# Kernel optimization log

Hardware: AMD Instinct MI355X
Metric: run time of the kernel (lower is better)

The kernel has to match this reference:

```python
import jax, jax.numpy as jnp
import numpy as np

EMBED_DIM = 1024
NUM_MEMORY_SLOTS = 256
B, Q = 8, 4096


def setup_inputs() -> dict:
    key = jax.random.key(0)
    ks = jax.random.split(key, 6)
    s = 1.0 / np.sqrt(EMBED_DIM)
    return {
        "x": jax.random.normal(ks[0], (B, Q, EMBED_DIM), dtype=jnp.float32),
        "memory_bank": jax.random.normal(ks[1], (NUM_MEMORY_SLOTS, EMBED_DIM), dtype=jnp.float32),
        "Wq": jax.random.uniform(ks[2], (EMBED_DIM, EMBED_DIM), jnp.float32, -s, s),
        "bq": jax.random.uniform(ks[3], (EMBED_DIM,), jnp.float32, -s, s),
        "Wo": jax.random.uniform(ks[4], (EMBED_DIM, EMBED_DIM), jnp.float32, -s, s),
        "bo": jax.random.uniform(ks[5], (EMBED_DIM,), jnp.float32, -s, s),
    }


def reference(x, memory_bank, Wq, bq, Wo, bo):
    # query projection: [B,Q,E]
    queries = jnp.einsum('bqe,fe->bqf', x, Wq) + bq
    # attention over fixed memory bank: scores [B,Q,M]
    scores = jnp.einsum('bqe,me->bqm', queries, memory_bank)
    weights = jax.nn.softmax(scores, axis=-1)
    attended = jnp.einsum('bqm,me->bqe', weights, memory_bank)
    # output projection + residual
    return jnp.einsum('bqe,fe->bqf', attended, Wo) + bo + x
```

## Files before the change

### kernel.cpp

```cpp
#include <hip/hip_runtime.h>
#include <hip/hip_bf16.h>
#include <stdint.h>

#define TOK 32768
#define EMB 1024
#define MSL 256

typedef __attribute__((ext_vector_type(8))) short short8;
typedef __attribute__((ext_vector_type(4))) float f32x4;

__device__ __forceinline__ ushort f2bf(float f) {
    union { float f; uint32_t u; } c; c.f = f;
    uint32_t u = c.u;
    return (ushort)((u + 0x7fffu + ((u >> 16) & 1u)) >> 16);
}

__device__ __forceinline__ void split2(float f, ushort& h, ushort& l) {
    union { float f; uint32_t u; } c; c.f = f;
    h = (ushort)(c.u >> 16);
    union { uint32_t u; float f; } hv; hv.u = c.u & 0xffff0000u;
    union { float f; uint32_t u; } lc; lc.f = f - hv.f;
    l = (ushort)(lc.u >> 16);
}

__device__ __forceinline__ void async_copy16(const void* gsrc, void* ldst) {
    __builtin_amdgcn_global_load_lds(
        (const __attribute__((address_space(1))) uint32_t*)gsrc,
        (__attribute__((address_space(3))) uint32_t*)ldst,
        16, 0, 0);
}


__global__ __launch_bounds__(256) void pre_small(
    const float* __restrict__ Wq, ushort* __restrict__ wqth, ushort* __restrict__ wqtl,
    const float* __restrict__ mb, ushort* __restrict__ mbh, ushort* __restrict__ mbl,
    const float* __restrict__ bq, float* __restrict__ cvec)
{
    __shared__ float ld[64 * 65];
    const int b = blockIdx.x;
    const int t = threadIdx.x;
    if (b < 256) {
        const int eBase = (b & 15) * 64;
        const int fBase = (b >> 4) * 64;
        #pragma unroll
        for (int r = 0; r < 16; ++r) {
            int row = r * 4 + (t >> 6);
            int col = t & 63;
            ld[row * 65 + col] = Wq[(size_t)(fBase + row) * EMB + eBase + col];
        }
        __syncthreads();
        #pragma unroll
        for (int r = 0; r < 16; ++r) {
            int row = r * 4 + (t >> 6);
            int col = t & 63;
            float v = ld[col * 65 + row];
            ushort h, l; split2(v, h, l);
            size_t o = (size_t)(eBase + row) * EMB + fBase + col;
            wqth[o] = h; wqtl[o] = l;
        }
    } else if (b < 512) {
        int i = (b - 256) * 256 + t;
        float4 v = ((const float4*)mb)[i];
        ushort4 h4, l4;
        split2(v.x, h4.x, l4.x); split2(v.y, h4.y, l4.y);
        split2(v.z, h4.z, l4.z); split2(v.w, h4.w, l4.w);
        ((ushort4*)mbh)[i] = h4;
        ((ushort4*)mbl)[i] = l4;
    } else {
        int m = (b - 512) * 4 + (t >> 6);
        int lane = t & 63;
        const float4* mrow = (const float4*)(mb + (size_t)m * EMB);
        const float4* brow = (const float4*)bq;
        float s = 0.f;
        #pragma unroll
        for (int k = 0; k < 4; ++k) {
            float4 a = mrow[lane + k * 64];
            float4 bb = brow[lane + k * 64];
            s += a.x * bb.x + a.y * bb.y + a.z * bb.z + a.w * bb.w;
        }
        #pragma unroll
        for (int off = 32; off; off >>= 1) s += __shfl_xor(s, off, 64);
        if (lane == 0) cvec[m] = s;
    }
}

template<int MODE>
__device__ __forceinline__ void gemm_body(
    ushort* smem, const float* __restrict__ A,
    const ushort* __restrict__ Bh, const ushort* __restrict__ Bl,
    ushort* __restrict__ O1, ushort* __restrict__ O2,
    int K, int ldc, int bx, int by)
{
    ushort* sAh = smem;
    ushort* sAl = smem + 8192;
    ushort* sBh = smem + 16384;
    ushort* sBl = smem + 24576;

    const int t = threadIdx.x;
    const int lane = t & 63;
    const int wave = t >> 6;
    const int wr = wave >> 1;
    const int wc = wave & 1;
    const int rowBase = by * 128;
    const int colBase = bx * 128;

    const float*  Ab  = A  + (size_t)rowBase * K;
    const ushort* Bhb = Bh + (size_t)colBase * K;
    const ushort* Blb = Bl + (size_t)colBase * K;

    const int cg = ((t & 7) ^ ((t >> 3) & 7)) << 3;

    f32x4 acc[4][4] = {};

    const int kIters = K >> 6;
    for (int kt = 0; kt < kIters; ++kt) {
        const int k0 = kt << 6;
        __syncthreads();
        #pragma unroll
        for (int r = 0; r < 4; ++r) {
            int row = r * 32 + (t >> 3);
            async_copy16(Bhb + (size_t)row * K + k0 + cg, &sBh[(size_t)(r * 256 + wave * 64) * 8]);
            async_copy16(Blb + (size_t)row * K + k0 + cg, &sBl[(size_t)(r * 256 + wave * 64) * 8]);
        }
        #pragma unroll
        for (int r = 0; r < 4; ++r) {
            int i = r * 256 + t;
            int row = r * 32 + (t >> 3);
            const float* src = Ab + (size_t)row * K + k0 + cg;
            float4 f0 = *(const float4*)src;
            float4 f1 = *(const float4*)(src + 4);
            short8 hv, lv; ushort h, l;
            split2(f0.x, h, l); hv[0] = (short)h; lv[0] = (short)l;
            split2(f0.y, h, l); hv[1] = (short)h; lv[1] = (short)l;
            split2(f0.z, h, l); hv[2] = (short)h; lv[2] = (short)l;
            split2(f0.w, h, l); hv[3] = (short)h; lv[3] = (short)l;
            split2(f1.x, h, l); hv[4] = (short)h; lv[4] = (short)l;
            split2(f1.y, h, l); hv[5] = (short)h; lv[5] = (short)l;
            split2(f1.z, h, l); hv[6] = (short)h; lv[6] = (short)l;
            split2(f1.w, h, l); hv[7] = (short)h; lv[7] = (short)l;
            *(short8*)&sAh[(size_t)i * 8] = hv;
            *(short8*)&sAl[(size_t)i * 8] = lv;
        }
        __syncthreads();

        #pragma unroll
        for (int ks = 0; ks < 2; ++ks) {
            const int kc = ks * 4 + (lane >> 4);
            short8 ah[4], al[4], bh[4], bl[4];
            #pragma unroll
            for (int i2 = 0; i2 < 4; ++i2) {
                int row = wr * 64 + i2 * 16 + (lane & 15);
                int off = row * 64 + ((kc ^ (row & 7)) << 3);
                ah[i2] = *(const short8*)&sAh[off];
                al[i2] = *(const short8*)&sAl[off];
            }
            #pragma unroll
            for (int j = 0; j < 4; ++j) {
                int row = wc * 64 + j * 16 + (lane & 15);
                int off = row * 64 + ((kc ^ (row & 7)) << 3);
                bh[j] = *(const short8*)&sBh[off];
                bl[j] = *(const short8*)&sBl[off];
            }
            #pragma unroll
            for (int i2 = 0; i2 < 4; ++i2)
                #pragma unroll
                for (int j = 0; j < 4; ++j) {
                    acc[i2][j] = __builtin_amdgcn_mfma_f32_16x16x32_bf16(ah[i2], bh[j], acc[i2][j], 0, 0, 0);
                    acc[i2][j] = __builtin_amdgcn_mfma_f32_16x16x32_bf16(ah[i2], bl[j], acc[i2][j], 0, 0, 0);
                    acc[i2][j] = __builtin_amdgcn_mfma_f32_16x16x32_bf16(al[i2], bh[j], acc[i2][j], 0, 0, 0);
                }
        }
    }

    #pragma unroll
    for (int i2 = 0; i2 < 4; ++i2) {
        #pragma unroll
        for (int j = 0; j < 4; ++j) {
            const int col = colBase + wc * 64 + j * 16 + (lane & 15);
            #pragma unroll
            for (int r = 0; r < 4; ++r) {
                const int row = rowBase + wr * 64 + i2 * 16 + ((lane >> 4) << 2) + r;
                float v = acc[i2][j][r];
                if (MODE == 0) {
                    ushort h, l; split2(v, h, l);
                    O1[(size_t)row * ldc + col] = h;
                    O2[(size_t)row * ldc + col] = l;
                } else {
                    int fc = row >> 6, jj = (row & 63) >> 4, lanelo = row & 15;
                    int cc = col >> 3, ksx = cc >> 2, lanehi = cc & 3, e = col & 7;
                    size_t idx = ((((size_t)fc * 8 + ksx) * 4 + jj) * 64 + lanehi * 16 + lanelo) * 8 + e;
                    O1[idx] = f2bf(v);
                }
            }
        }
    }
}

__global__ __launch_bounds__(256) void pre_gemms(
    const float* __restrict__ mb, const ushort* __restrict__ wqth, const ushort* __restrict__ wqtl,
    const float* __restrict__ Wo, const ushort* __restrict__ mbh, const ushort* __restrict__ mbl,
    ushort* __restrict__ Ph, ushort* __restrict__ Pl, ushort* __restrict__ RTfrag)
{
    __shared__ ushort smem[32768];
    const int b = blockIdx.x;
    if (b < 16) {
        gemm_body<0>(smem, mb, wqth, wqtl, Ph, Pl, EMB, EMB, b & 7, b >> 3);
    } else {
        const int id = b - 16;
        gemm_body<1>(smem, Wo, mbh, mbl, RTfrag, nullptr, EMB, 0, id & 1, id >> 1);
    }
}

__global__ __launch_bounds__(256, 2) void fused_attn(
    const float* __restrict__ x, const ushort* __restrict__ Ph,
    const ushort* __restrict__ Pl, const float* __restrict__ cvec,
    const ushort* __restrict__ RTfrag, const float* __restrict__ bo,
    float* __restrict__ out)
{
    __shared__ ushort smem[40960];
    ushort* sAh = smem;
    ushort* sAl = smem + 4096;
    ushort* sBh = smem + 8192;
    ushort* sBl = smem + 24576;
    ushort* sW  = smem;
    float*  redM = (float*)&smem[39936];
    float*  redS = (float*)&smem[40448];

    const int t = threadIdx.x;
    const int lane = t & 63;
    const int wave = t >> 6;
    const int wc = wave;
    const int rowBase = blockIdx.x * 64;

    const float* Ab = x + (size_t)rowBase * EMB;
    const int cg = ((t & 7) ^ ((t >> 3) & 7)) << 3;

    f32x4 acc[4][4] = {};

    for (int kt = 0; kt < 16; ++kt) {
        const int k0 = kt << 6;
        __syncthreads();
        #pragma unroll
        for (int r = 0; r < 8; ++r) {
            int row = r * 32 + (t >> 3);
            async_copy16(Ph + (size_t)row * EMB + k0 + cg, &sBh[(size_t)(r * 256 + wave * 64) * 8]);
            async_copy16(Pl + (size_t)row * EMB + k0 + cg, &sBl[(size_t)(r * 256 + wave * 64) * 8]);
        }
        #pragma unroll
        for (int r = 0; r < 2; ++r) {
            int i = r * 256 + t;
            int row = r * 32 + (t >> 3);
            const float* src = Ab + (size_t)row * EMB + k0 + cg;
            float4 f0 = *(const float4*)src;
            float4 f1 = *(const float4*)(src + 4);
            short8 hv, lv; ushort h, l;
            split2(f0.x, h, l); hv[0] = (short)h; lv[0] = (short)l;
            split2(f0.y, h, l); hv[1] = (short)h; lv[1] = (short)l;
            split2(f0.z, h, l); hv[2] = (short)h; lv[2] = (short)l;
            split2(f0.w, h, l); hv[3] = (short)h; lv[3] = (short)l;
            split2(f1.x, h, l); hv[4] = (short)h; lv[4] = (short)l;
            split2(f1.y, h, l); hv[5] = (short)h; lv[5] = (short)l;
            split2(f1.z, h, l); hv[6] = (short)h; lv[6] = (short)l;
            split2(f1.w, h, l); hv[7] = (short)h; lv[7] = (short)l;
            *(short8*)&sAh[(size_t)i * 8] = hv;
            *(short8*)&sAl[(size_t)i * 8] = lv;
        }
        __syncthreads();

        #pragma unroll
        for (int ks = 0; ks < 2; ++ks) {
            const int kc = ks * 4 + (lane >> 4);
            short8 ah[4], al[4], bh[4], bl[4];
            #pragma unroll
            for (int i2 = 0; i2 < 4; ++i2) {
                int row = i2 * 16 + (lane & 15);
                int off = row * 64 + ((kc ^ (row & 7)) << 3);
                ah[i2] = *(const short8*)&sAh[off];
                al[i2] = *(const short8*)&sAl[off];
            }
            #pragma unroll
            for (int j = 0; j < 4; ++j) {
                int row = wc * 64 + j * 16 + (lane & 15);
                int off = row * 64 + ((kc ^ (row & 7)) << 3);
                bh[j] = *(const short8*)&sBh[off];
                bl[j] = *(const short8*)&sBl[off];
            }
            #pragma unroll
            for (int i2 = 0; i2 < 4; ++i2)
                #pragma unroll
                for (int j = 0; j < 4; ++j) {
                    acc[i2][j] = __builtin_amdgcn_mfma_f32_16x16x32_bf16(ah[i2], bh[j], acc[i2][j], 0, 0, 0);
                    acc[i2][j] = __builtin_amdgcn_mfma_f32_16x16x32_bf16(ah[i2], bl[j], acc[i2][j], 0, 0, 0);
                    acc[i2][j] = __builtin_amdgcn_mfma_f32_16x16x32_bf16(al[i2], bh[j], acc[i2][j], 0, 0, 0);
                }
        }
    }

    {
        float cj[4];
        #pragma unroll
        for (int j = 0; j < 4; ++j) cj[j] = cvec[wc * 64 + j * 16 + (lane & 15)];
        #pragma unroll
        for (int i2 = 0; i2 < 4; ++i2)
            #pragma unroll
            for (int j = 0; j < 4; ++j)
                #pragma unroll
                for (int r = 0; r < 4; ++r) acc[i2][j][r] += cj[j];
    }
    float pmax[4][4];
    #pragma unroll
    for (int i2 = 0; i2 < 4; ++i2)
        #pragma unroll
        for (int r = 0; r < 4; ++r) {
            float m0 = fmaxf(fmaxf(acc[i2][0][r], acc[i2][1][r]),
                             fmaxf(acc[i2][2][r], acc[i2][3][r]));
            #pragma unroll
            for (int off = 8; off; off >>= 1) m0 = fmaxf(m0, __shfl_xor(m0, off, 64));
            pmax[i2][r] = m0;
        }
    __syncthreads();
    if ((lane & 15) == 0) {
        #pragma unroll
        for (int i2 = 0; i2 < 4; ++i2)
            #pragma unroll
            for (int r = 0; r < 4; ++r)
                redM[wc * 64 + i2 * 16 + ((lane >> 4) << 2) + r] = pmax[i2][r];
    }
    __syncthreads();
    {
        float psum[4][4];
        #pragma unroll
        for (int i2 = 0; i2 < 4; ++i2)
            #pragma unroll
            for (int r = 0; r < 4; ++r) {
                int R = i2 * 16 + ((lane >> 4) << 2) + r;
                float mx = fmaxf(fmaxf(redM[R], redM[64 + R]),
                                 fmaxf(redM[128 + R], redM[192 + R]));
                float s = 0.f;
                #pragma unroll
                for (int j = 0; j < 4; ++j) {
                    float e = __expf(acc[i2][j][r] - mx);
                    acc[i2][j][r] = e;
                    s += e;
                }
                #pragma unroll
                for (int off = 8; off; off >>= 1) s += __shfl_xor(s, off, 64);
                psum[i2][r] = s;
            }
        if ((lane & 15) == 0) {
            #pragma unroll
            for (int i2 = 0; i2 < 4; ++i2)
                #pragma unroll
                for (int r = 0; r < 4; ++r)
                    redS[wc * 64 + i2 * 16 + ((lane >> 4) << 2) + r] = psum[i2][r];
        }
    }
    __syncthreads();
    #pragma unroll
    for (int i2 = 0; i2 < 4; ++i2)
        #pragma unroll
        for (int r = 0; r < 4; ++r) {
            int R = i2 * 16 + ((lane >> 4) << 2) + r;
            float tot = redS[R] + redS[64 + R] + redS[128 + R] + redS[192 + R];
            float inv = 1.0f / tot;
            #pragma unroll
            for (int j = 0; j < 4; ++j) {
                int col = wc * 64 + j * 16 + (lane & 15);
                int cc = col >> 3;
                int slot = (cc & 24) | ((cc & 7) ^ (R & 7));
                sW[R * 256 + slot * 8 + (lane & 7)] = f2bf(acc[i2][j][r] * inv);
            }
        }
    __syncthreads();

    const int wr2 = wave >> 1;
    const int wc2 = wave & 1;

    short8 af[2][8];
    #pragma unroll
    for (int i2 = 0; i2 < 2; ++i2) {
        int R = wr2 * 32 + i2 * 16 + (lane & 15);
        #pragma unroll
        for (int ks = 0; ks < 8; ++ks) {
            int cc = ks * 4 + (lane >> 4);
            int slot = (cc & 24) | ((cc & 7) ^ (R & 7));
            af[i2][ks] = *(const short8*)&sW[R * 256 + slot * 8];
        }
    }

    for (int fc = 0; fc < 16; ++fc) {
        f32x4 acc2[2][2] = {};
        #pragma unroll
        for (int ks = 0; ks < 8; ++ks) {
            short8 b[2];
            #pragma unroll
            for (int j = 0; j < 2; ++j) {
                int jj = wc2 * 2 + j;
                b[j] = *(const short8*)&RTfrag[((((size_t)fc * 8 + ks) * 4 + jj) * 64 + lane) * 8];
            }
            #pragma unroll
            for (int i2 = 0; i2 < 2; ++i2)
                #pragma unroll
                for (int j = 0; j < 2; ++j)
                    acc2[i2][j] = __builtin_amdgcn_mfma_f32_16x16x32_bf16(
                        af[i2][ks], b[j], acc2[i2][j], 0, 0, 0);
        }
        #pragma unroll
        for (int i2 = 0; i2 < 2; ++i2)
            #pragma unroll
            for (int j = 0; j < 2; ++j) {
                int col = fc * 64 + wc2 * 32 + j * 16 + (lane & 15);
                float bcol = bo[col];
                #pragma unroll
                for (int r = 0; r < 4; ++r) {
                    int row = rowBase + wr2 * 32 + i2 * 16 + ((lane >> 4) << 2) + r;
                    out[(size_t)row * EMB + col] =
                        acc2[i2][j][r] + bcol + x[(size_t)row * EMB + col];
                }
            }
    }
}

extern "C" void kernel_launch(void* const* d_in, const int* in_sizes, int n_in,
                              void* d_out, int out_size, void* d_ws, size_t ws_size,
                              hipStream_t stream) {
    const float* x  = (const float*)d_in[0];
    const float* mb = (const float*)d_in[1];
    const float* Wq = (const float*)d_in[2];
    const float* bq = (const float*)d_in[3];
    const float* Wo = (const float*)d_in[4];
    const float* bo = (const float*)d_in[5];
    float* out = (float*)d_out;

    char* ws = (char*)d_ws;
    size_t o = 0;
    ushort* mbh    = (ushort*)(ws + o); o += (size_t)MSL * EMB * 2;
    ushort* mbl    = (ushort*)(ws + o); o += (size_t)MSL * EMB * 2;
    ushort* wqth   = (ushort*)(ws + o); o += (size_t)EMB * EMB * 2;
    ushort* wqtl   = (ushort*)(ws + o); o += (size_t)EMB * EMB * 2;
    ushort* Ph     = (ushort*)(ws + o); o += (size_t)MSL * EMB * 2;
    ushort* Pl     = (ushort*)(ws + o); o += (size_t)MSL * EMB * 2;
    ushort* RTfrag = (ushort*)(ws + o); o += (size_t)EMB * MSL * 2;
    float*  cvec   = (float*)(ws + o);  o += (size_t)MSL * 4;

    pre_small<<<576, 256, 0, stream>>>(Wq, wqth, wqtl, mb, mbh, mbl, bq, cvec);

    pre_gemms<<<32, 256, 0, stream>>>(mb, wqth, wqtl, Wo, mbh, mbl, Ph, Pl, RTfrag);

    fused_attn<<<TOK / 64, 256, 0, stream>>>(x, Ph, Pl, cvec, RTfrag, bo, out);
}
```

Baseline: 350.7 us.

## Double-buffer P tiles and prefetch x with larger 128-row blocks

The fused attention kernel now processes 128 rows per block with 512 threads in a 2x4 wave grid, instead of 64 rows with 256 threads. This halves how often each block must reload the projected memory bank P. The P tiles are double-buffered in LDS through async global-to-LDS copies issued one k-step ahead. The next x tile is also prefetched into registers while the current one is computed. LDS use grows to about 160KB, so only one block fits per CU, and the extra prefetch registers may push up register pressure.

```diff
diff --git a/kernel.cpp b/kernel.cpp
--- a/kernel.cpp
+++ b/kernel.cpp
@@ -8,6 +8,8 @@
 
 typedef __attribute__((ext_vector_type(8))) short short8;
 typedef __attribute__((ext_vector_type(4))) float f32x4;
+
+#define SBAR() asm volatile("s_waitcnt lgkmcnt(0)\n\ts_barrier" ::: "memory")
 
 __device__ __forceinline__ ushort f2bf(float f) {
     union { float f; uint32_t u; } c; c.f = f;
@@ -211,69 +213,88 @@
     }
 }
 
-__global__ __launch_bounds__(256, 2) void fused_attn(
+__global__ __launch_bounds__(512, 2) void fused_attn(
     const float* __restrict__ x, const ushort* __restrict__ Ph,
     const ushort* __restrict__ Pl, const float* __restrict__ cvec,
     const ushort* __restrict__ RTfrag, const float* __restrict__ bo,
     float* __restrict__ out)
 {
-    __shared__ ushort smem[40960];
+    __shared__ ushort smem[81920];
     ushort* sAh = smem;
-    ushort* sAl = smem + 4096;
-    ushort* sBh = smem + 8192;
-    ushort* sBl = smem + 24576;
-    ushort* sW  = smem;
-    float*  redM = (float*)&smem[39936];
-    float*  redS = (float*)&smem[40448];
+    ushort* sAl = smem + 8192;
+    ushort* sW  = smem + 16384;
+    float*  redM = (float*)&smem[0];
+    float*  redS = (float*)&smem[1024];
 
     const int t = threadIdx.x;
     const int lane = t & 63;
     const int wave = t >> 6;
-    const int wc = wave;
-    const int rowBase = blockIdx.x * 64;
+    const int wr = wave >> 2;
+    const int wc = wave & 3;
+    const int rowBase = blockIdx.x * 128;
 
     const float* Ab = x + (size_t)rowBase * EMB;
     const int cg = ((t & 7) ^ ((t >> 3) & 7)) << 3;
 
     f32x4 acc[4][4] = {};
+    float4 xr[2][2];
+
+    auto stageB = [&](int kt, ushort* bb) {
+        const int k0 = kt << 6;
+        ushort* bh = bb;
+        ushort* bl = bb + 16384;
+        #pragma unroll
+        for (int r = 0; r < 4; ++r) {
+            int row = r * 64 + (t >> 3);
+            async_copy16(Ph + (size_t)row * EMB + k0 + cg, &bh[(size_t)(r * 512 + wave * 64) * 8]);
+            async_copy16(Pl + (size_t)row * EMB + k0 + cg, &bl[(size_t)(r * 512 + wave * 64) * 8]);
+        }
+    };
+    auto loadX = [&](int kt) {
+        const int k0 = kt << 6;
+        #pragma unroll
+        for (int r = 0; r < 2; ++r) {
+            const float* src = Ab + (size_t)(r * 64 + (t >> 3)) * EMB + k0 + cg;
+            xr[r][0] = *(const float4*)src;
+            xr[r][1] = *(const float4*)(src + 4);
+        }
+    };
+
+    stageB(0, smem + 16384);
+    loadX(0);
 
     for (int kt = 0; kt < 16; ++kt) {
-        const int k0 = kt << 6;
-        __syncthreads();
-        #pragma unroll
-        for (int r = 0; r < 8; ++r) {
-            int row = r * 32 + (t >> 3);
-            async_copy16(Ph + (size_t)row * EMB + k0 + cg, &sBh[(size_t)(r * 256 + wave * 64) * 8]);
-            async_copy16(Pl + (size_t)row * EMB + k0 + cg, &sBl[(size_t)(r * 256 + wave * 64) * 8]);
-        }
+        SBAR();
         #pragma unroll
         for (int r = 0; r < 2; ++r) {
-            int i = r * 256 + t;
-            int row = r * 32 + (t >> 3);
-            const float* src = Ab + (size_t)row * EMB + k0 + cg;
-            float4 f0 = *(const float4*)src;
-            float4 f1 = *(const float4*)(src + 4);
+            int i = r * 512 + t;
             short8 hv, lv; ushort h, l;
-            split2(f0.x, h, l); hv[0] = (short)h; lv[0] = (short)l;
-            split2(f0.y, h, l); hv[1] = (short)h; lv[1] = (short)l;
-            split2(f0.z, h, l); hv[2] = (short)h; lv[2] = (short)l;
-            split2(f0.w, h, l); hv[3] = (short)h; lv[3] = (short)l;
-            split2(f1.x, h, l); hv[4] = (short)h; lv[4] = (short)l;
-            split2(f1.y, h, l); hv[5] = (short)h; lv[5] = (short)l;
-            split2(f1.z, h, l); hv[6] = (short)h; lv[6] = (short)l;
-            split2(f1.w, h, l); hv[7] = (short)h; lv[7] = (short)l;
+            split2(xr[r][0].x, h, l); hv[0] = (short)h; lv[0] = (short)l;
+            split2(xr[r][0].y, h, l); hv[1] = (short)h; lv[1] = (short)l;
+            split2(xr[r][0].z, h, l); hv[2] = (short)h; lv[2] = (short)l;
+            split2(xr[r][0].w, h, l); hv[3] = (short)h; lv[3] = (short)l;
+            split2(xr[r][1].x, h, l); hv[4] = (short)h; lv[4] = (short)l;
+            split2(xr[r][1].y, h, l); hv[5] = (short)h; lv[5] = (short)l;
+            split2(xr[r][1].z, h, l); hv[6] = (short)h; lv[6] = (short)l;
+            split2(xr[r][1].w, h, l); hv[7] = (short)h; lv[7] = (short)l;
             *(short8*)&sAh[(size_t)i * 8] = hv;
             *(short8*)&sAl[(size_t)i * 8] = lv;
         }
-        __syncthreads();
-
+        if (kt < 15) {
+            stageB(kt + 1, ((kt + 1) & 1) ? (smem + 49152) : (smem + 16384));
+            loadX(kt + 1);
+        }
+        SBAR();
+
+        const ushort* cbh = (kt & 1) ? (smem + 49152) : (smem + 16384);
+        const ushort* cbl = cbh + 16384;
         #pragma unroll
         for (int ks = 0; ks < 2; ++ks) {
             const int kc = ks * 4 + (lane >> 4);
             short8 ah[4], al[4], bh[4], bl[4];
             #pragma unroll
             for (int i2 = 0; i2 < 4; ++i2) {
-                int row = i2 * 16 + (lane & 15);
+                int row = wr * 64 + i2 * 16 + (lane & 15);
                 int off = row * 64 + ((kc ^ (row & 7)) << 3);
                 ah[i2] = *(const short8*)&sAh[off];
                 al[i2] = *(const short8*)&sAl[off];
@@ -282,8 +303,8 @@
             for (int j = 0; j < 4; ++j) {
                 int row = wc * 64 + j * 16 + (lane & 15);
                 int off = row * 64 + ((kc ^ (row & 7)) << 3);
-                bh[j] = *(const short8*)&sBh[off];
-                bl[j] = *(const short8*)&sBl[off];
+                bh[j] = *(const short8*)&cbh[off];
+                bl[j] = *(const short8*)&cbl[off];
             }
             #pragma unroll
             for (int i2 = 0; i2 < 4; ++i2)
@@ -324,7 +345,7 @@
         for (int i2 = 0; i2 < 4; ++i2)
             #pragma unroll
             for (int r = 0; r < 4; ++r)
-                redM[wc * 64 + i2 * 16 + ((lane >> 4) << 2) + r] = pmax[i2][r];
+                redM[wc * 128 + wr * 64 + i2 * 16 + ((lane >> 4) << 2) + r] = pmax[i2][r];
     }
     __syncthreads();
     {
@@ -333,9 +354,9 @@
         for (int i2 = 0; i2 < 4; ++i2)
             #pragma unroll
             for (int r = 0; r < 4; ++r) {
-                int R = i2 * 16 + ((lane >> 4) << 2) + r;
-                float mx = fmaxf(fmaxf(redM[R], redM[64 + R]),
-                                 fmaxf(redM[128 + R], redM[192 + R]));
+                int R = wr * 64 + i2 * 16 + ((lane >> 4) << 2) + r;
+                float mx = fmaxf(fmaxf(redM[R], redM[128 + R]),
+                                 fmaxf(redM[256 + R], redM[384 + R]));
                 float s = 0.f;
                 #pragma unroll
                 for (int j = 0; j < 4; ++j) {
@@ -352,7 +373,7 @@
             for (int i2 = 0; i2 < 4; ++i2)
                 #pragma unroll
                 for (int r = 0; r < 4; ++r)
-                    redS[wc * 64 + i2 * 16 + ((lane >> 4) << 2) + r] = psum[i2][r];
+                    redS[wc * 128 + wr * 64 + i2 * 16 + ((lane >> 4) << 2) + r] = psum[i2][r];
         }
     }
     __syncthreads();
@@ -360,8 +381,8 @@
     for (int i2 = 0; i2 < 4; ++i2)
         #pragma unroll
         for (int r = 0; r < 4; ++r) {
-            int R = i2 * 16 + ((lane >> 4) << 2) + r;
-            float tot = redS[R] + redS[64 + R] + redS[128 + R] + redS[192 + R];
+            int R = wr * 64 + i2 * 16 + ((lane >> 4) << 2) + r;
+            float tot = redS[R] + redS[128 + R] + redS[256 + R] + redS[384 + R];
             float inv = 1.0f / tot;
             #pragma unroll
             for (int j = 0; j < 4; ++j) {
@@ -447,5 +468,5 @@
 
     pre_gemms<<<32, 256, 0, stream>>>(mb, wqth, wqtl, Wo, mbh, mbl, Ph, Pl, RTfrag);
 
-    fused_attn<<<TOK / 64, 256, 0, stream>>>(x, Ph, Pl, cvec, RTfrag, bo, out);
-}
+    fused_attn<<<TOK / 128, 512, 0, stream>>>(x, Ph, Pl, cvec, RTfrag, bo, out);
+}
```

Result: no change. 352.5 us (+0.5%).

## Read projected memory B-fragments directly from global in MFMA layout, double-buffer x tile

Applied to the files above, without the earlier changes.

The pre-GEMM now writes the projected memory bank (hi/lo bf16 split) in an MFMA-fragment-ordered layout. This lets the fused attention kernel load B operands straight from global/L2 as contiguous 16-byte per-lane reads instead of staging them through LDS. LDS use drops enough to raise launch bounds to 3 blocks per CU. The x tile is register-prefetched one k-step ahead and written into double-buffered LDS, with a single barrier per iteration. The trade-off is more global/L2 traffic per block for the B operand and higher register pressure from the prefetch.

```diff
diff --git a/kernel.cpp b/kernel.cpp
--- a/kernel.cpp
+++ b/kernel.cpp
@@ -8,6 +8,8 @@
 
 typedef __attribute__((ext_vector_type(8))) short short8;
 typedef __attribute__((ext_vector_type(4))) float f32x4;
+
+#define SBAR() asm volatile("s_waitcnt lgkmcnt(0)\n\ts_barrier" ::: "memory")
 
 __device__ __forceinline__ ushort f2bf(float f) {
     union { float f; uint32_t u; } c; c.f = f;
@@ -89,7 +91,7 @@
     ushort* smem, const float* __restrict__ A,
     const ushort* __restrict__ Bh, const ushort* __restrict__ Bl,
     ushort* __restrict__ O1, ushort* __restrict__ O2,
-    int K, int ldc, int bx, int by)
+    int K, int bx, int by)
 {
     ushort* sAh = smem;
     ushort* sAl = smem + 8192;
@@ -182,9 +184,13 @@
                 const int row = rowBase + wr * 64 + i2 * 16 + ((lane >> 4) << 2) + r;
                 float v = acc[i2][j][r];
                 if (MODE == 0) {
+                    int ktx = col >> 6, kcc = (col >> 3) & 7;
+                    int ksx = kcc >> 2, lh = kcc & 3, e = col & 7;
+                    int wcj = row >> 4, ll = row & 15;
+                    size_t idx = (((size_t)(ktx * 2 + ksx) * 16 + wcj) * 64 + lh * 16 + ll) * 8 + e;
                     ushort h, l; split2(v, h, l);
-                    O1[(size_t)row * ldc + col] = h;
-                    O2[(size_t)row * ldc + col] = l;
+                    O1[idx] = h;
+                    O2[idx] = l;
                 } else {
                     int fc = row >> 6, jj = (row & 63) >> 4, lanelo = row & 15;
                     int cc = col >> 3, ksx = cc >> 2, lanehi = cc & 3, e = col & 7;
@@ -199,32 +205,28 @@
 __global__ __launch_bounds__(256) void pre_gemms(
     const float* __restrict__ mb, const ushort* __restrict__ wqth, const ushort* __restrict__ wqtl,
     const float* __restrict__ Wo, const ushort* __restrict__ mbh, const ushort* __restrict__ mbl,
-    ushort* __restrict__ Ph, ushort* __restrict__ Pl, ushort* __restrict__ RTfrag)
+    ushort* __restrict__ Pfh, ushort* __restrict__ Pfl, ushort* __restrict__ RTfrag)
 {
     __shared__ ushort smem[32768];
     const int b = blockIdx.x;
     if (b < 16) {
-        gemm_body<0>(smem, mb, wqth, wqtl, Ph, Pl, EMB, EMB, b & 7, b >> 3);
+        gemm_body<0>(smem, mb, wqth, wqtl, Pfh, Pfl, EMB, b & 7, b >> 3);
     } else {
         const int id = b - 16;
-        gemm_body<1>(smem, Wo, mbh, mbl, RTfrag, nullptr, EMB, 0, id & 1, id >> 1);
-    }
-}
-
-__global__ __launch_bounds__(256, 2) void fused_attn(
-    const float* __restrict__ x, const ushort* __restrict__ Ph,
-    const ushort* __restrict__ Pl, const float* __restrict__ cvec,
+        gemm_body<1>(smem, Wo, mbh, mbl, RTfrag, nullptr, EMB, id & 1, id >> 1);
+    }
+}
+
+__global__ __launch_bounds__(256, 3) void fused_attn(
+    const float* __restrict__ x, const ushort* __restrict__ Pfh,
+    const ushort* __restrict__ Pfl, const float* __restrict__ cvec,
     const ushort* __restrict__ RTfrag, const float* __restrict__ bo,
     float* __restrict__ out)
 {
-    __shared__ ushort smem[40960];
-    ushort* sAh = smem;
-    ushort* sAl = smem + 4096;
-    ushort* sBh = smem + 8192;
-    ushort* sBl = smem + 24576;
+    __shared__ ushort smem[17408];
     ushort* sW  = smem;
-    float*  redM = (float*)&smem[39936];
-    float*  redS = (float*)&smem[40448];
+    float*  redM = (float*)&smem[16384];
+    float*  redS = (float*)&smem[16896];
 
     const int t = threadIdx.x;
     const int lane = t & 63;
@@ -236,36 +238,40 @@
     const int cg = ((t & 7) ^ ((t >> 3) & 7)) << 3;
 
     f32x4 acc[4][4] = {};
+    float4 xr[2][2];
+
+    auto loadX = [&](int kt) {
+        const int k0 = kt << 6;
+        #pragma unroll
+        for (int r = 0; r < 2; ++r) {
+            const float* src = Ab + (size_t)(r * 32 + (t >> 3)) * EMB + k0 + cg;
+            xr[r][0] = *(const float4*)src;
+            xr[r][1] = *(const float4*)(src + 4);
+        }
+    };
+
+    loadX(0);
 
     for (int kt = 0; kt < 16; ++kt) {
-        const int k0 = kt << 6;
-        __syncthreads();
-        #pragma unroll
-        for (int r = 0; r < 8; ++r) {
-            int row = r * 32 + (t >> 3);
-            async_copy16(Ph + (size_t)row * EMB + k0 + cg, &sBh[(size_t)(r * 256 + wave * 64) * 8]);
-            async_copy16(Pl + (size_t)row * EMB + k0 + cg, &sBl[(size_t)(r * 256 + wave * 64) * 8]);
-        }
+        ushort* bufAh = smem + (kt & 1) * 8192;
+        ushort* bufAl = bufAh + 4096;
         #pragma unroll
         for (int r = 0; r < 2; ++r) {
             int i = r * 256 + t;
-            int row = r * 32 + (t >> 3);
-            const float* src = Ab + (size_t)row * EMB + k0 + cg;
-            float4 f0 = *(const float4*)src;
-            float4 f1 = *(const float4*)(src + 4);
             short8 hv, lv; ushort h, l;
-            split2(f0.x, h, l); hv[0] = (short)h; lv[0] = (short)l;
-            split2(f0.y, h, l); hv[1] = (short)h; lv[1] = (short)l;
-            split2(f0.z, h, l); hv[2] = (short)h; lv[2] = (short)l;
-            split2(f0.w, h, l); hv[3] = (short)h; lv[3] = (short)l;
-            split2(f1.x, h, l); hv[4] = (short)h; lv[4] = (short)l;
-            split2(f1.y, h, l); hv[5] = (short)h; lv[5] = (short)l;
-            split2(f1.z, h, l); hv[6] = (short)h; lv[6] = (short)l;
-            split2(f1.w, h, l); hv[7] = (short)h; lv[7] = (short)l;
-            *(short8*)&sAh[(size_t)i * 8] = hv;
-            *(short8*)&sAl[(size_t)i * 8] = lv;
-        }
-        __syncthreads();
+            split2(xr[r][0].x, h, l); hv[0] = (short)h; lv[0] = (short)l;
+            split2(xr[r][0].y, h, l); hv[1] = (short)h; lv[1] = (short)l;
+            split2(xr[r][0].z, h, l); hv[2] = (short)h; lv[2] = (short)l;
+            split2(xr[r][0].w, h, l); hv[3] = (short)h; lv[3] = (short)l;
+            split2(xr[r][1].x, h, l); hv[4] = (short)h; lv[4] = (short)l;
+            split2(xr[r][1].y, h, l); hv[5] = (short)h; lv[5] = (short)l;
+            split2(xr[r][1].z, h, l); hv[6] = (short)h; lv[6] = (short)l;
+            split2(xr[r][1].w, h, l); hv[7] = (short)h; lv[7] = (short)l;
+            *(short8*)&bufAh[(size_t)i * 8] = hv;
+            *(short8*)&bufAl[(size_t)i * 8] = lv;
+        }
+        if (kt < 15) loadX(kt + 1);
+        SBAR();
 
         #pragma unroll
         for (int ks = 0; ks < 2; ++ks) {
@@ -275,15 +281,14 @@
             for (int i2 = 0; i2 < 4; ++i2) {
                 int row = i2 * 16 + (lane & 15);
                 int off = row * 64 + ((kc ^ (row & 7)) << 3);
-                ah[i2] = *(const short8*)&sAh[off];
-                al[i2] = *(const short8*)&sAl[off];
+                ah[i2] = *(const short8*)&bufAh[off];
+                al[i2] = *(const short8*)&bufAl[off];
             }
             #pragma unroll
             for (int j = 0; j < 4; ++j) {
-                int row = wc * 64 + j * 16 + (lane & 15);
-                int off = row * 64 + ((kc ^ (row & 7)) << 3);
-                bh[j] = *(const short8*)&sBh[off];
-                bl[j] = *(const short8*)&sBl[off];
+                size_t boff = ((size_t)((kt * 2 + ks) * 16 + wc * 4 + j) * 64 + lane) * 8;
+                bh[j] = *(const short8*)&Pfh[boff];
+                bl[j] = *(const short8*)&Pfl[boff];
             }
             #pragma unroll
             for (int i2 = 0; i2 < 4; ++i2)
@@ -438,14 +443,14 @@
     ushort* mbl    = (ushort*)(ws + o); o += (size_t)MSL * EMB * 2;
     ushort* wqth   = (ushort*)(ws + o); o += (size_t)EMB * EMB * 2;
     ushort* wqtl   = (ushort*)(ws + o); o += (size_t)EMB * EMB * 2;
-    ushort* Ph     = (ushort*)(ws + o); o += (size_t)MSL * EMB * 2;
-    ushort* Pl     = (ushort*)(ws + o); o += (size_t)MSL * EMB * 2;
+    ushort* Pfh    = (ushort*)(ws + o); o += (size_t)MSL * EMB * 2;
+    ushort* Pfl    = (ushort*)(ws + o); o += (size_t)MSL * EMB * 2;
     ushort* RTfrag = (ushort*)(ws + o); o += (size_t)EMB * MSL * 2;
     float*  cvec   = (float*)(ws + o);  o += (size_t)MSL * 4;
 
     pre_small<<<576, 256, 0, stream>>>(Wq, wqth, wqtl, mb, mbh, mbl, bq, cvec);
 
-    pre_gemms<<<32, 256, 0, stream>>>(mb, wqth, wqtl, Wo, mbh, mbl, Ph, Pl, RTfrag);
-
-    fused_attn<<<TOK / 64, 256, 0, stream>>>(x, Ph, Pl, cvec, RTfrag, bo, out);
-}
+    pre_gemms<<<32, 256, 0, stream>>>(mb, wqth, wqtl, Wo, mbh, mbl, Pfh, Pfl, RTfrag);
+
+    fused_attn<<<TOK / 64, 256, 0, stream>>>(x, Pfh, Pfl, cvec, RTfrag, bo, out);
+}
```

Result: slower. 368.5 us (+5.1%).
